# Performance work log

Hardware: AMD Instinct MI355X
Metric: run time of the kernel (lower is better)

## Reference

```python
import jax, jax.numpy as jnp
import numpy as np

NEG = 0.01  # leaky_relu negative slope

def leaky(x):
    return jax.nn.leaky_relu(x, NEG)

def mlp3(x, W0, b0, W1, b1, W2, b2):
    h = leaky(x @ W0 + b0)
    h = leaky(h @ W1 + b1)
    return h @ W2 + b2

B_, T_, N_FINE, F_IN = 2, 4, 64800, 78
N_COARSE, E_LAT, H, D_OUT = 842, 5894, 256, 256

def setup_inputs() -> dict:
    key = jax.random.key(0)
    ks = jax.random.split(key, 24)
    def lin(k, i, o):
        return jax.random.normal(k, (i, o), jnp.float32) * 0.02, jnp.zeros((o,), jnp.float32)
    x = jax.random.normal(ks[0], (B_, T_, N_FINE, F_IN), jnp.float32)
    # one edge per fine node: src = node index, dst = its coarse h3 cell
    edge_index = jnp.stack([jnp.arange(N_FINE, dtype=jnp.int32),
                            jax.random.randint(ks[1], (N_FINE,), 0, N_COARSE, dtype=jnp.int32)])
    edge_attr = 2.0 * jax.random.uniform(ks[2], (N_FINE, 2), jnp.float32) - 1.0  # [sin d, cos d]
    latent_edge_index = jax.random.randint(ks[3], (2, E_LAT), 0, N_COARSE, dtype=jnp.int32)
    latent_edge_attr = 2.0 * jax.random.uniform(ks[4], (E_LAT, 2), jnp.float32) - 1.0
    h3_nodes = jax.random.normal(ks[5], (N_COARSE, F_IN), jnp.float32) * 0.02
    eW0, eb0 = lin(ks[6], 2 * F_IN + 2, H); eW1, eb1 = lin(ks[7], H, H); eW2, eb2 = lin(ks[8], H, D_OUT)
    nW0, nb0 = lin(ks[9], F_IN + D_OUT, H); nW1, nb1 = lin(ks[10], H, H); nW2, nb2 = lin(ks[11], H, D_OUT)
    rW0, rb0 = lin(ks[12], 2, H); rW1, rb1 = lin(ks[13], H, H); rW2, rb2 = lin(ks[14], H, D_OUT)
    rWs, rbs = lin(ks[15], 2, D_OUT)
    return dict(x=x, edge_index=edge_index, edge_attr=edge_attr,
                latent_edge_index=latent_edge_index, latent_edge_attr=latent_edge_attr,
                h3_nodes=h3_nodes,
                eW0=eW0, eb0=eb0, eW1=eW1, eb1=eb1, eW2=eW2, eb2=eb2,
                nW0=nW0, nb0=nb0, nW1=nW1, nb1=nb1, nW2=nW2, nb2=nb2,
                rW0=rW0, rb0=rb0, rW1=rW1, rb1=rb1, rW2=rW2, rb2=rb2,
                rWs=rWs, rbs=rbs)

def reference(x, edge_index, edge_attr, latent_edge_index, latent_edge_attr, h3_nodes,
              eW0, eb0, eW1, eb1, eW2, eb2,
              nW0, nb0, nW1, nb1, nW2, nb2,
              rW0, rb0, rW1, rb1, rW2, rb2, rWs, rbs):
    b, t, n, f = x.shape
    B = b * t
    xf = x.reshape(B, n, f)                      # (b t) n f
    src, dst = edge_index[0], edge_index[1]      # [E]
    nc = h3_nodes.shape[0]
    E = src.shape[0]
    # --- edge MLP: gather src fine feats, dst latent feats, edge attrs ---
    e_in = jnp.concatenate([
        xf[:, src],                                          # [B,E,f]
        jnp.broadcast_to(h3_nodes[dst][None], (B, E, f)),    # [B,E,f]
        jnp.broadcast_to(edge_attr[None], (B, E, 2)),        # [B,E,2]
    ], axis=-1)
    msgs = mlp3(e_in, eW0, eb0, eW1, eb1, eW2, eb2)          # [B,E,D]
    # --- scatter-sum to coarse nodes ---
    agg = jax.vmap(lambda m: jax.ops.segment_sum(m, dst, num_segments=nc))(msgs)  # [B,nc,D]
    # --- node MLP on concat(latent nodes, aggregated messages) ---
    n_in = jnp.concatenate([jnp.broadcast_to(h3_nodes[None], (B, nc, f)), agg], axis=-1)
    nodes = mlp3(n_in, nW0, nb0, nW1, nb1, nW2, nb2)          # [B,nc,D]
    nodes = nodes.reshape(b, t, nc, -1)
    # --- residual MLP over latent edge attrs (eval: dropout off, parametrized skip) ---
    h = leaky(latent_edge_attr @ rW0 + rb0)
    h = leaky(h @ rW1 + rb1)
    attrs = h @ rW2 + rb2 + (latent_edge_attr @ rWs + rbs)
    return (nodes, latent_edge_index, attrs)
```

## Files before the change

### kernel.cpp

```cpp
#include <hip/hip_runtime.h>

#define E_EDGES 64800
#define NC      842
#define NB      8
#define FIN     78
#define E_LAT   5894
#define NROWS_NODE (NB*NC)
#define NTILES_E 1350

#define OUT_IDX_OFF   1724416
#define OUT_IDX_N     11788
#define OUT_ATTR_OFF  1736204

#define AGG_OFF    0
#define CNT_OFF    6897664
#define CUR_OFF    6901032
#define SSRC_OFF   6904400
#define SDST_OFF   7163600
#define SATTR_OFF  7293200
#define WPACK_OFF  7811600

#define WOFF_E0 0
#define WOFF_E1 40960
#define WOFF_E2 106496
#define WOFF_N0 172032
#define WOFF_N1 262144
#define WOFF_N2 327680
#define WOFF_R0 393216
#define WOFF_R1 401408
#define WOFF_R2 466944

#define SH   262
#define SA_N 362

typedef __bf16 bf16x8 __attribute__((ext_vector_type(8)));
typedef float  f32x4  __attribute__((ext_vector_type(4)));

__device__ __forceinline__ unsigned short f2bf(float f) {
    unsigned u = __builtin_bit_cast(unsigned, f);
    return (unsigned short)((u + 0x7fffu + ((u >> 16) & 1u)) >> 16);
}
__device__ __forceinline__ unsigned packRTZ(float lo, float hi) {
    return __builtin_amdgcn_perm(__builtin_bit_cast(unsigned, hi),
                                 __builtin_bit_cast(unsigned, lo), 0x07060302u);
}

template<int MF>
__device__ __forceinline__ void zero_acc(f32x4 (&acc)[MF][4]) {
#pragma unroll
    for (int mf = 0; mf < MF; ++mf)
#pragma unroll
        for (int nf = 0; nf < 4; ++nf)
            acc[mf][nf] = (f32x4){0.f, 0.f, 0.f, 0.f};
}

template<int MF, int NKS>
__device__ __forceinline__ void run_layer(const unsigned short* lA, int strideA,
                                          const unsigned short* Wp, int nfg0,
                                          int m15, int q, f32x4 (&acc)[MF][4]) {
    const unsigned short* wp0 = Wp + (size_t)nfg0 * 512 + (threadIdx.x & 63) * 8;
    const unsigned short* a0 = lA + m15 * strideA + q * 8;
    bf16x8 bcur[4], bnxt[4], acur[MF], anxt[MF];
#pragma unroll
    for (int nf = 0; nf < 4; ++nf) bcur[nf] = *(const bf16x8*)(wp0 + nf * 512);
#pragma unroll
    for (int mf = 0; mf < MF; ++mf) acur[mf] = *(const bf16x8*)(a0 + mf * 16 * strideA);
#pragma unroll
    for (int kk = 0; kk < NKS; ++kk) {
        if (kk + 1 < NKS) {
#pragma unroll
            for (int nf = 0; nf < 4; ++nf)
                bnxt[nf] = *(const bf16x8*)(wp0 + (size_t)(kk + 1) * 16 * 512 + nf * 512);
#pragma unroll
            for (int mf = 0; mf < MF; ++mf)
                anxt[mf] = *(const bf16x8*)(a0 + mf * 16 * strideA + (kk + 1) * 32);
        }
#pragma unroll
        for (int nf = 0; nf < 4; ++nf)
#pragma unroll
            for (int mf = 0; mf < MF; ++mf)
                acc[mf][nf] = __builtin_amdgcn_mfma_f32_16x16x32_bf16(acur[mf], bcur[nf], acc[mf][nf], 0, 0, 0);
#pragma unroll
        for (int nf = 0; nf < 4; ++nf) bcur[nf] = bnxt[nf];
#pragma unroll
        for (int mf = 0; mf < MF; ++mf) acur[mf] = anxt[mf];
    }
}

template<int MF>
__device__ __forceinline__ void epi_act(unsigned short* Sb, int stride, const f32x4 (&acc)[MF][4],
                                        const float* bias, int w, int m15, int q) {
#pragma unroll
    for (int nf = 0; nf < 4; ++nf) {
        int col = w * 64 + nf * 16 + m15;
        float bv = bias[col];
#pragma unroll
        for (int mf = 0; mf < MF; ++mf)
#pragma unroll
            for (int r4 = 0; r4 < 4; ++r4) {
                int row = mf * 16 + q * 4 + r4;
                float y = acc[mf][nf][r4] + bv;
                y = fmaxf(y, 0.01f * y);
                Sb[row * stride + col] = (unsigned short)(__builtin_bit_cast(unsigned, y) >> 16);
            }
    }
}

__global__ void pack_weights(const float* s0, const float* s1, const float* s2,
                             const float* s3, const float* s4, const float* s5,
                             const float* s6, const float* s7, const float* s8,
                             unsigned short* wp) {
    const int ksA[9]  = {5, 8, 8, 11, 8, 8, 1, 8, 8};
    const int kaA[9]  = {158, 256, 256, 334, 256, 256, 2, 256, 256};
    const int offA[9] = {WOFF_E0, WOFF_E1, WOFF_E2, WOFF_N0, WOFF_N1, WOFF_N2,
                         WOFF_R0, WOFF_R1, WOFF_R2};
    const float* srcs[9] = {s0, s1, s2, s3, s4, s5, s6, s7, s8};
    int rem = blockIdx.x;
    int l = 0;
    while (rem >= ksA[l] * 16) { rem -= ksA[l] * 16; ++l; }
    int kk = rem >> 4, nf = rem & 15;
    int lane = threadIdx.x >> 3, j = threadIdx.x & 7;
    int k = kk * 32 + (lane >> 4) * 8 + j;
    int n = nf * 16 + (lane & 15);
    float v = (k < kaA[l]) ? srcs[l][k * 256 + n] : 0.f;
    wp[(size_t)offA[l] + (size_t)(kk * 16 + nf) * 512 + lane * 8 + j] = f2bf(v);
}

__global__ void hist_kernel(const int* __restrict__ dstA, int* __restrict__ cnt) {
    int e = blockIdx.x * 256 + threadIdx.x;
    if (e < E_EDGES) atomicAdd(&cnt[dstA[e]], 1);
}
__global__ void scan_kernel(const int* __restrict__ cnt, int* __restrict__ cursor) {
    __shared__ int s[1024];
    int t = threadIdx.x;
    s[t] = (t < NC) ? cnt[t] : 0;
    __syncthreads();
    for (int d = 1; d < 1024; d <<= 1) {
        int v = (t >= d) ? s[t - d] : 0;
        __syncthreads();
        s[t] += v;
        __syncthreads();
    }
    if (t < NC) cursor[t] = (t == 0) ? 0 : s[t - 1];
}
__global__ void scatter_kernel(const int* __restrict__ srcA, const int* __restrict__ dstA,
                               const float* __restrict__ eattr, int* __restrict__ cursor,
                               int* __restrict__ ssrc, short* __restrict__ sdst,
                               float2* __restrict__ sattr) {
    int e = blockIdx.x * 256 + threadIdx.x;
    if (e < E_EDGES) {
        int d = dstA[e];
        int p = atomicAdd(&cursor[d], 1);
        ssrc[p] = srcA[e];
        sdst[p] = (short)d;
        sattr[p] = ((const float2*)eattr)[e];
    }
}

__global__ __launch_bounds__(256, 4) void edge_mlp_kernel(
    const float* __restrict__ x, const float* __restrict__ h3,
    const float* __restrict__ eb0, const float* __restrict__ eb1, const float* __restrict__ eb2,
    const unsigned short* __restrict__ wpack, const int* __restrict__ ssrc,
    const short* __restrict__ sdst, const float2* __restrict__ sattr,
    float* __restrict__ agg) {
    __shared__ __align__(16) unsigned short S[48 * SH];
    __shared__ short dstl[48];
    __shared__ unsigned char starts[52];
    __shared__ int nseg;

    const int base = blockIdx.x * 48, b = blockIdx.y;
    const int tid = threadIdx.x, lane = tid & 63, w = tid >> 6;
    const int m15 = lane & 15, q = lane >> 4;

    if (tid < 48) dstl[tid] = sdst[base + tid];
    __syncthreads();

    if (tid == 0) {
        int ns = 0; short prev = -2;
        for (int r = 0; r < 48; ++r) {
            short d = dstl[r];
            if (d != prev) { starts[ns++] = (unsigned char)r; prev = d; }
        }
        starts[ns] = 48;
        nseg = ns;
    }

    {
        const int rr = tid >> 3, j = tid & 7;
#pragma unroll
        for (int pass = 0; pass < 2; ++pass) {
            const int row = pass * 32 + rr;
            if (pass == 0 || tid < 128) {
                const int eg = base + row;
                const float* xr = x + ((size_t)b * E_EDGES + ssrc[eg]) * FIN;
                const float* hr = h3 + (int)dstl[row] * FIN;
                unsigned short* Sr = S + row * SH;
#pragma unroll
                for (int t = 0; t < 5; ++t) {
                    int p = j + 8 * t;
                    if (p < 39) {
                        float2 f = *(const float2*)(xr + 2 * p);
                        float2 g = *(const float2*)(hr + 2 * p);
                        *(unsigned*)(Sr + 2 * p) = packRTZ(f.x, f.y);
                        *(unsigned*)(Sr + 78 + 2 * p) = packRTZ(g.x, g.y);
                    } else if (p == 39) {
                        float2 a2 = sattr[eg];
                        *(unsigned*)(Sr + 156) = packRTZ(a2.x, a2.y);
                        *(unsigned*)(Sr + 158) = 0;
                    }
                }
            }
        }
    }
    float bnf[4];
#pragma unroll
    for (int nf = 0; nf < 4; ++nf) bnf[nf] = eb2[w * 64 + nf * 16 + m15];
    __syncthreads();

    f32x4 acc[3][4];
    zero_acc<3>(acc);
    run_layer<3, 5>(S, SH, wpack + WOFF_E0, w * 4, m15, q, acc);
    __syncthreads();
    epi_act<3>(S, SH, acc, eb0, w, m15, q);
    __syncthreads();

    zero_acc<3>(acc);
    run_layer<3, 8>(S, SH, wpack + WOFF_E1, w * 4, m15, q, acc);
    __syncthreads();
    epi_act<3>(S, SH, acc, eb1, w, m15, q);
    __syncthreads();

    zero_acc<3>(acc);
    run_layer<3, 8>(S, SH, wpack + WOFF_E2, w * 4, m15, q, acc);

    const int ns = nseg;
#pragma unroll
    for (int nf = 0; nf < 4; ++nf) {
        for (int s = 0; s < ns; ++s) {
            const int lo = starts[s], hi = starts[s + 1];
            float t = 0.f;
#pragma unroll
            for (int mf = 0; mf < 3; ++mf)
#pragma unroll
                for (int r4 = 0; r4 < 4; ++r4) {
                    int row = mf * 16 + q * 4 + r4;
                    t += (row >= lo && row < hi) ? acc[mf][nf][r4] : 0.f;
                }
            t += __shfl_xor(t, 16, 64);
            t += __shfl_xor(t, 32, 64);
            if (q == nf) {
                int dc = dstl[lo];
                atomicAdd(&agg[((size_t)b * NC + dc) * 256 + w * 64 + nf * 16 + m15],
                          t + bnf[nf] * (float)(hi - lo));
            }
        }
    }
}

__global__ __launch_bounds__(256, 4) void node_mlp_kernel(
    const float* __restrict__ h3, const float* __restrict__ agg,
    const float* __restrict__ nb0, const float* __restrict__ nb1, const float* __restrict__ nb2,
    const unsigned short* __restrict__ wpack, float* __restrict__ out) {
    __shared__ __align__(16) unsigned short S[16 * SA_N];

    const int base = blockIdx.x * 16;
    const int tid = threadIdx.x, lane = tid & 63, w = tid >> 6;
    const int m15 = lane & 15, q = lane >> 4;

    {
        const int rr = tid >> 4, l16 = tid & 15;
        const int jj = base + rr;
        const int vl = jj < NROWS_NODE;
        const int c = vl ? jj % NC : 0;
        const float* hr = h3 + c * FIN;
        const float* ar = agg + (size_t)jj * 256;
        unsigned short* Sr = S + rr * SA_N;
#pragma unroll
        for (int t = 0; t < 12; ++t) {
            int p = l16 + 16 * t;
            if (p < 39) {
                float2 f = *(const float2*)(hr + 2 * p);
                *(unsigned*)(Sr + 2 * p) = packRTZ(f.x, f.y);
            } else if (p < 167) {
                unsigned v = 0;
                if (vl) { float2 f = *(const float2*)(ar + 2 * p - 78); v = packRTZ(f.x, f.y); }
                *(unsigned*)(Sr + 2 * p) = v;
            } else if (p < 176) {
                *(unsigned*)(Sr + 2 * p) = 0;
            }
        }
    }
    __syncthreads();

    f32x4 acc[1][4];
    zero_acc<1>(acc);
    run_layer<1, 11>(S, SA_N, wpack + WOFF_N0, w * 4, m15, q, acc);
    __syncthreads();
    epi_act<1>(S, SA_N, acc, nb0, w, m15, q);
    __syncthreads();

    zero_acc<1>(acc);
    run_layer<1, 8>(S, SA_N, wpack + WOFF_N1, w * 4, m15, q, acc);
    __syncthreads();
    epi_act<1>(S, SA_N, acc, nb1, w, m15, q);
    __syncthreads();

    zero_acc<1>(acc);
    run_layer<1, 8>(S, SA_N, wpack + WOFF_N2, w * 4, m15, q, acc);

#pragma unroll
    for (int nf = 0; nf < 4; ++nf) {
        int col = w * 64 + nf * 16 + m15;
        float bv = nb2[col];
#pragma unroll
        for (int r4 = 0; r4 < 4; ++r4) {
            int jj = base + q * 4 + r4;
            if (jj < NROWS_NODE) out[(size_t)jj * 256 + col] = acc[0][nf][r4] + bv;
        }
    }
}

__global__ __launch_bounds__(256, 4) void tail_kernel(
    const float* __restrict__ la, const float* __restrict__ rb0, const float* __restrict__ rb1,
    const float* __restrict__ rb2, const float* __restrict__ rWs, const float* __restrict__ rbs,
    const unsigned short* __restrict__ wpack, const int* __restrict__ lei,
    float* __restrict__ out) {
    __shared__ __align__(16) unsigned short S[32 * SH];

    const int blk = blockIdx.x;
    const int tid = threadIdx.x;
    if (blk >= 185) {
        for (int i = (blk - 185) * 256 + tid; i < OUT_IDX_N; i += 7 * 256)
            out[OUT_IDX_OFF + i] = (float)lei[i];
        return;
    }

    const int base = blk * 32;
    const int lane = tid & 63, w = tid >> 6;
    const int m15 = lane & 15, q = lane >> 4;

    {
        const int rr = tid >> 3, j = tid & 7;
        unsigned short* Sr = S + rr * SH;
        unsigned v0 = 0;
        if (j == 0 && base + rr < E_LAT) {
            float2 f = *(const float2*)(la + (size_t)(base + rr) * 2);
            v0 = packRTZ(f.x, f.y);
        }
        *(unsigned*)(Sr + 2 * j) = v0;
        *(unsigned*)(Sr + 2 * (j + 8)) = 0;
    }
    __syncthreads();

    f32x4 acc[2][4];
    zero_acc<2>(acc);
    run_layer<2, 1>(S, SH, wpack + WOFF_R0, w * 4, m15, q, acc);
    __syncthreads();
    epi_act<2>(S, SH, acc, rb0, w, m15, q);
    __syncthreads();

    zero_acc<2>(acc);
    run_layer<2, 8>(S, SH, wpack + WOFF_R1, w * 4, m15, q, acc);
    __syncthreads();
    epi_act<2>(S, SH, acc, rb1, w, m15, q);
    __syncthreads();

    zero_acc<2>(acc);
    run_layer<2, 8>(S, SH, wpack + WOFF_R2, w * 4, m15, q, acc);

    float* outA = out + OUT_ATTR_OFF;
#pragma unroll
    for (int nf = 0; nf < 4; ++nf) {
        int col = w * 64 + nf * 16 + m15;
        float bv = rb2[col] + rbs[col];
        float ws0 = rWs[col], ws1 = rWs[256 + col];
#pragma unroll
        for (int mf = 0; mf < 2; ++mf)
#pragma unroll
            for (int r4 = 0; r4 < 4; ++r4) {
                int row = mf * 16 + q * 4 + r4;
                int e = base + row;
                if (e < E_LAT) {
                    float v = acc[mf][nf][r4] + bv + la[e * 2] * ws0 + la[e * 2 + 1] * ws1;
                    outA[(size_t)e * 256 + col] = v;
                }
            }
    }
}

extern "C" void kernel_launch(void* const* d_in, const int* in_sizes, int n_in,
                              void* d_out, int out_size, void* d_ws, size_t ws_size,
                              hipStream_t stream) {
    const float* x      = (const float*)d_in[0];
    const int*   eidx   = (const int*)d_in[1];
    const float* eattr  = (const float*)d_in[2];
    const int*   lei    = (const int*)d_in[3];
    const float* la     = (const float*)d_in[4];
    const float* h3     = (const float*)d_in[5];
    const float* eW0 = (const float*)d_in[6],  *eb0 = (const float*)d_in[7];
    const float* eW1 = (const float*)d_in[8],  *eb1 = (const float*)d_in[9];
    const float* eW2 = (const float*)d_in[10], *eb2 = (const float*)d_in[11];
    const float* nW0 = (const float*)d_in[12], *nb0 = (const float*)d_in[13];
    const float* nW1 = (const float*)d_in[14], *nb1 = (const float*)d_in[15];
    const float* nW2 = (const float*)d_in[16], *nb2 = (const float*)d_in[17];
    const float* rW0 = (const float*)d_in[18], *rb0 = (const float*)d_in[19];
    const float* rW1 = (const float*)d_in[20], *rb1 = (const float*)d_in[21];
    const float* rW2 = (const float*)d_in[22], *rb2 = (const float*)d_in[23];
    const float* rWs = (const float*)d_in[24], *rbs = (const float*)d_in[25];

    char* ws = (char*)d_ws;
    float* agg    = (float*)(ws + AGG_OFF);
    int* cnt      = (int*)(ws + CNT_OFF);
    int* cur      = (int*)(ws + CUR_OFF);
    int* ssrc     = (int*)(ws + SSRC_OFF);
    short* sdst   = (short*)(ws + SDST_OFF);
    float2* sattr = (float2*)(ws + SATTR_OFF);
    unsigned short* wpack = (unsigned short*)(ws + WPACK_OFF);

    float* out = (float*)d_out;

    hipMemsetAsync(d_ws, 0, CUR_OFF, stream);

    pack_weights<<<1040, 512, 0, stream>>>(eW0, eW1, eW2, nW0, nW1, nW2, rW0, rW1, rW2, wpack);
    hist_kernel<<<254, 256, 0, stream>>>(eidx + E_EDGES, cnt);
    scan_kernel<<<1, 1024, 0, stream>>>(cnt, cur);
    scatter_kernel<<<254, 256, 0, stream>>>(eidx, eidx + E_EDGES, eattr, cur,
                                            ssrc, sdst, sattr);
    tail_kernel<<<192, 256, 0, stream>>>(la, rb0, rb1, rb2, rWs, rbs, wpack, lei, out);
    edge_mlp_kernel<<<dim3(NTILES_E, NB), 256, 0, stream>>>(x, h3, eb0, eb1, eb2,
                                                            wpack, ssrc, sdst, sattr, agg);
    node_mlp_kernel<<<421, 256, 0, stream>>>(h3, agg, nb0, nb1, nb2, wpack, out);
}
```

Baseline: 706.8 us.

## Stage edge-MLP weights into a double-buffered LDS ring and enlarge edge tiles

The edge MLP kernel now streams each 32-wide K-slice of the weight matrices into a two-slot LDS ring with global_load_lds DMA, prefetching two steps ahead and running across layer boundaries. Row tiles grow from 48 to 80 edges (810 tiles), so each weight fetch feeds more MFMAs. Occupancy drops from 4 to 2 blocks per CU, and the kernel relies on hand-placed vmcnt waits for correctness. The generic run_layer also stops prefetching A fragments and loads them just before use, which reduces register pressure.

```diff
diff --git a/kernel.cpp b/kernel.cpp
--- a/kernel.cpp
+++ b/kernel.cpp
@@ -6,7 +6,7 @@
 #define FIN     78
 #define E_LAT   5894
 #define NROWS_NODE (NB*NC)
-#define NTILES_E 1350
+#define NTILES_E 810
 
 #define OUT_IDX_OFF   1724416
 #define OUT_IDX_N     11788
@@ -30,6 +30,8 @@
 #define WOFF_R1 401408
 #define WOFF_R2 466944
 
+#define WSTEP 8192
+
 #define SH   262
 #define SA_N 362
 
@@ -45,6 +47,15 @@
                                  __builtin_bit_cast(unsigned, lo), 0x07060302u);
 }
 
+typedef const unsigned int __attribute__((address_space(1)))* gas1_t;
+typedef unsigned int __attribute__((address_space(3)))* las3_t;
+__device__ __forceinline__ void gld_lds16(const unsigned short* g, unsigned short* l) {
+    __builtin_amdgcn_global_load_lds((gas1_t)(unsigned long long)g,
+                                     (las3_t)(unsigned)(unsigned long long)l, 16, 0, 0);
+}
+__device__ __forceinline__ void wait_vm4() { asm volatile("s_waitcnt vmcnt(4)" ::: "memory"); }
+__device__ __forceinline__ void wait_vm0() { asm volatile("s_waitcnt vmcnt(0)" ::: "memory"); }
+
 template<int MF>
 __device__ __forceinline__ void zero_acc(f32x4 (&acc)[MF][4]) {
 #pragma unroll
@@ -52,6 +63,44 @@
 #pragma unroll
         for (int nf = 0; nf < 4; ++nf)
             acc[mf][nf] = (f32x4){0.f, 0.f, 0.f, 0.f};
+}
+
+template<int MF, int NKS, int P, bool HN>
+__device__ __forceinline__ void run_layer_dma(const unsigned short* lA, int strideA,
+                                              unsigned short* Br,
+                                              const unsigned short* Wg,
+                                              const unsigned short* WgN,
+                                              int w, int m15, int q,
+                                              f32x4 (&acc)[MF][4]) {
+    const int lane8 = (threadIdx.x & 63) * 8;
+#pragma unroll
+    for (int kk = 0; kk < NKS; ++kk) {
+        bf16x8 a[MF];
+#pragma unroll
+        for (int mf = 0; mf < MF; ++mf)
+            a[mf] = *(const bf16x8*)(lA + (mf * 16 + m15) * strideA + kk * 32 + q * 8);
+        if (HN || kk < NKS - 1) wait_vm4(); else wait_vm0();
+        const unsigned short* bs = Br + ((P + kk) & 1) * WSTEP + w * 2048 + lane8;
+        bf16x8 b[4];
+#pragma unroll
+        for (int nf = 0; nf < 4; ++nf) b[nf] = *(const bf16x8*)(bs + nf * 512);
+        const int t = kk + 2;
+        const unsigned short* src = (t < NKS) ? (Wg + (size_t)t * WSTEP)
+                                  : (HN && (t - NKS) < 2) ? (WgN + (size_t)(t - NKS) * WSTEP)
+                                  : (const unsigned short*)0;
+        if (src) {
+            unsigned short* dst = Br + ((P + t) & 1) * WSTEP + w * 2048;
+            const unsigned short* s2 = src + w * 2048 + lane8;
+#pragma unroll
+            for (int i = 0; i < 4; ++i)
+                gld_lds16(s2 + i * 512, dst + i * 512);
+        }
+#pragma unroll
+        for (int nf = 0; nf < 4; ++nf)
+#pragma unroll
+            for (int mf = 0; mf < MF; ++mf)
+                acc[mf][nf] = __builtin_amdgcn_mfma_f32_16x16x32_bf16(a[mf], b[nf], acc[mf][nf], 0, 0, 0);
+    }
 }
 
 template<int MF, int NKS>
@@ -60,30 +109,27 @@
                                           int m15, int q, f32x4 (&acc)[MF][4]) {
     const unsigned short* wp0 = Wp + (size_t)nfg0 * 512 + (threadIdx.x & 63) * 8;
     const unsigned short* a0 = lA + m15 * strideA + q * 8;
-    bf16x8 bcur[4], bnxt[4], acur[MF], anxt[MF];
+    bf16x8 bcur[4], bnxt[4];
 #pragma unroll
     for (int nf = 0; nf < 4; ++nf) bcur[nf] = *(const bf16x8*)(wp0 + nf * 512);
-#pragma unroll
-    for (int mf = 0; mf < MF; ++mf) acur[mf] = *(const bf16x8*)(a0 + mf * 16 * strideA);
 #pragma unroll
     for (int kk = 0; kk < NKS; ++kk) {
         if (kk + 1 < NKS) {
 #pragma unroll
             for (int nf = 0; nf < 4; ++nf)
                 bnxt[nf] = *(const bf16x8*)(wp0 + (size_t)(kk + 1) * 16 * 512 + nf * 512);
+        }
+        bf16x8 a[MF];
+#pragma unroll
+        for (int mf = 0; mf < MF; ++mf)
+            a[mf] = *(const bf16x8*)(a0 + mf * 16 * strideA + kk * 32);
+#pragma unroll
+        for (int nf = 0; nf < 4; ++nf)
 #pragma unroll
             for (int mf = 0; mf < MF; ++mf)
-                anxt[mf] = *(const bf16x8*)(a0 + mf * 16 * strideA + (kk + 1) * 32);
-        }
-#pragma unroll
-        for (int nf = 0; nf < 4; ++nf)
-#pragma unroll
-            for (int mf = 0; mf < MF; ++mf)
-                acc[mf][nf] = __builtin_amdgcn_mfma_f32_16x16x32_bf16(acur[mf], bcur[nf], acc[mf][nf], 0, 0, 0);
+                acc[mf][nf] = __builtin_amdgcn_mfma_f32_16x16x32_bf16(a[mf], bcur[nf], acc[mf][nf], 0, 0, 0);
 #pragma unroll
         for (int nf = 0; nf < 4; ++nf) bcur[nf] = bnxt[nf];
-#pragma unroll
-        for (int mf = 0; mf < MF; ++mf) acur[mf] = anxt[mf];
     }
 }
 
@@ -157,40 +203,51 @@
     }
 }
 
-__global__ __launch_bounds__(256, 4) void edge_mlp_kernel(
+__global__ __launch_bounds__(256, 2) void edge_mlp_kernel(
     const float* __restrict__ x, const float* __restrict__ h3,
     const float* __restrict__ eb0, const float* __restrict__ eb1, const float* __restrict__ eb2,
     const unsigned short* __restrict__ wpack, const int* __restrict__ ssrc,
     const short* __restrict__ sdst, const float2* __restrict__ sattr,
     float* __restrict__ agg) {
-    __shared__ __align__(16) unsigned short S[48 * SH];
-    __shared__ short dstl[48];
-    __shared__ unsigned char starts[52];
+    __shared__ __align__(16) unsigned short S[80 * SH];
+    __shared__ __align__(16) unsigned short Bring[2 * WSTEP];
+    __shared__ short dstl[80];
+    __shared__ unsigned char starts[84];
     __shared__ int nseg;
 
-    const int base = blockIdx.x * 48, b = blockIdx.y;
+    const int base = blockIdx.x * 80, b = blockIdx.y;
     const int tid = threadIdx.x, lane = tid & 63, w = tid >> 6;
     const int m15 = lane & 15, q = lane >> 4;
 
-    if (tid < 48) dstl[tid] = sdst[base + tid];
+    {
+        const unsigned short* s0 = wpack + WOFF_E0 + w * 2048 + lane * 8;
+        unsigned short* d0 = Bring + w * 2048;
+#pragma unroll
+        for (int t = 0; t < 2; ++t)
+#pragma unroll
+            for (int i = 0; i < 4; ++i)
+                gld_lds16(s0 + t * WSTEP + i * 512, d0 + t * WSTEP + i * 512);
+    }
+
+    if (tid < 80) dstl[tid] = sdst[base + tid];
     __syncthreads();
 
     if (tid == 0) {
         int ns = 0; short prev = -2;
-        for (int r = 0; r < 48; ++r) {
+        for (int r = 0; r < 80; ++r) {
             short d = dstl[r];
             if (d != prev) { starts[ns++] = (unsigned char)r; prev = d; }
         }
-        starts[ns] = 48;
+        starts[ns] = 80;
         nseg = ns;
     }
 
     {
         const int rr = tid >> 3, j = tid & 7;
 #pragma unroll
-        for (int pass = 0; pass < 2; ++pass) {
+        for (int pass = 0; pass < 3; ++pass) {
             const int row = pass * 32 + rr;
-            if (pass == 0 || tid < 128) {
+            if (pass < 2 || tid < 128) {
                 const int eg = base + row;
                 const float* xr = x + ((size_t)b * E_EDGES + ssrc[eg]) * FIN;
                 const float* hr = h3 + (int)dstl[row] * FIN;
@@ -217,21 +274,24 @@
     for (int nf = 0; nf < 4; ++nf) bnf[nf] = eb2[w * 64 + nf * 16 + m15];
     __syncthreads();
 
-    f32x4 acc[3][4];
-    zero_acc<3>(acc);
-    run_layer<3, 5>(S, SH, wpack + WOFF_E0, w * 4, m15, q, acc);
-    __syncthreads();
-    epi_act<3>(S, SH, acc, eb0, w, m15, q);
-    __syncthreads();
-
-    zero_acc<3>(acc);
-    run_layer<3, 8>(S, SH, wpack + WOFF_E1, w * 4, m15, q, acc);
-    __syncthreads();
-    epi_act<3>(S, SH, acc, eb1, w, m15, q);
-    __syncthreads();
-
-    zero_acc<3>(acc);
-    run_layer<3, 8>(S, SH, wpack + WOFF_E2, w * 4, m15, q, acc);
+    f32x4 acc[5][4];
+    zero_acc<5>(acc);
+    run_layer_dma<5, 5, 0, true>(S, SH, Bring, wpack + WOFF_E0, wpack + WOFF_E1,
+                                 w, m15, q, acc);
+    __syncthreads();
+    epi_act<5>(S, SH, acc, eb0, w, m15, q);
+    __syncthreads();
+
+    zero_acc<5>(acc);
+    run_layer_dma<5, 8, 1, true>(S, SH, Bring, wpack + WOFF_E1, wpack + WOFF_E2,
+                                 w, m15, q, acc);
+    __syncthreads();
+    epi_act<5>(S, SH, acc, eb1, w, m15, q);
+    __syncthreads();
+
+    zero_acc<5>(acc);
+    run_layer_dma<5, 8, 1, false>(S, SH, Bring, wpack + WOFF_E2, (const unsigned short*)0,
+                                  w, m15, q, acc);
 
     const int ns = nseg;
 #pragma unroll
@@ -240,7 +300,7 @@
             const int lo = starts[s], hi = starts[s + 1];
             float t = 0.f;
 #pragma unroll
-            for (int mf = 0; mf < 3; ++mf)
+            for (int mf = 0; mf < 5; ++mf)
 #pragma unroll
                 for (int r4 = 0; r4 < 4; ++r4) {
                     int row = mf * 16 + q * 4 + r4;
```

Result: slower. 828.0 us (+17.1%).
